# Kernel tuning notes

Measured on AMD Instinct MI355X. Metric: run time of the kernel, lower is better.

The kernel has to match this reference:

```python
import jax, jax.numpy as jnp
import numpy as np
import math

B, C, BINS, W = 2, 8, 1024, 512
HEADS = 16
HD = BINS // HEADS          # 64 head dim
ROT = BINS // HEADS // 2    # 32 rotated dims
EXP = 4
EPS = 1e-5
MAX_FREQ = 10.0


def setup_inputs() -> dict:
    key = jax.random.key(0)
    ks = jax.random.split(key, 8)
    def u(k, shape, fan_in):
        lim = 1.0 / math.sqrt(fan_in)
        return jax.random.uniform(k, shape, jnp.float32, -lim, lim)
    return {
        "x": jax.random.normal(ks[0], (B, C, BINS, W), jnp.float32),
        "norm1_w": jnp.ones((BINS,), jnp.float32),
        "norm1_b": jnp.zeros((BINS,), jnp.float32),
        # 'pixel' rotary init: linspace(1, max_freq/2, dim//2) * pi (learned)
        "rot_freqs": jnp.linspace(1.0, MAX_FREQ / 2, ROT // 2, dtype=jnp.float32) * math.pi,
        "q_w": u(ks[1], (C, BINS, BINS), BINS),
        "out_w": u(ks[2], (C, BINS, BINS), BINS),
        "norm2_w": jnp.ones((BINS,), jnp.float32),
        "norm2_b": jnp.zeros((BINS,), jnp.float32),
        "lin1_w": u(ks[3], (C, BINS * EXP, BINS), BINS),
        "lin2_w": u(ks[4], (C, BINS, BINS * EXP), BINS * EXP),
    }


def _mlin(x, w):
    # x: [b,c,f_in,w]; w: [c,f_out,f_in] -> [b,c,f_out,w]
    return jnp.einsum('bcfw,cgf->bcgw', x, w)


def _frame_norm(x, w, b):
    # LayerNorm over the bins axis (axis=2) of [b,c,bins,w]
    m = jnp.mean(x, axis=2, keepdims=True)
    v = jnp.var(x, axis=2, keepdims=True)
    xn = (x - m) * jax.lax.rsqrt(v + EPS)
    return xn * w[:, None] + b[:, None]


def _rotate(q, cos, sin):
    # q: [b,c,h,w,d]; rotate first ROT dims with interleaved-pair rotate_half
    q1, q2 = q[..., :ROT], q[..., ROT:]
    qp = q1.reshape(*q1.shape[:-1], ROT // 2, 2)
    rh = jnp.stack([-qp[..., 1], qp[..., 0]], axis=-1).reshape(q1.shape)
    return jnp.concatenate([q1 * cos + rh * sin, q2], axis=-1)


def _attention(x, rot_freqs, q_w, out_w):
    b, c, bins, w = x.shape
    # faithful to source: q, k, v ALL use q_proj
    y = _mlin(x, q_w)  # [b,c,bins,w]
    # -> [b,c,h,w,d]
    y = y.transpose(0, 1, 3, 2).reshape(b, c, w, HEADS, HD).transpose(0, 1, 3, 2, 4)
    # rotary angles: t * freqs, repeat-interleaved x2 -> [w, ROT]
    t = jnp.arange(w, dtype=jnp.float32)
    ang = jnp.repeat(t[:, None] * rot_freqs[None, :], 2, axis=-1)
    cos, sin = jnp.cos(ang), jnp.sin(ang)
    q = _rotate(y, cos, sin)
    k = _rotate(y, cos, sin)
    v = y
    # NOTE: source scales by 1/sqrt(h) where h == bins (spectral height)
    scores = jnp.einsum('bchwd,bchud->bchwu', q, k) / math.sqrt(bins)
    a = jnp.einsum('bchwu,bchud->bchwd', jax.nn.softmax(scores, axis=-1), v)
    # [b,c,h,w,d] -> [b,c,bins,w]
    a = a.transpose(0, 1, 3, 2, 4).reshape(b, c, w, bins).transpose(0, 1, 3, 2)
    return _mlin(a, out_w)


def reference(x, norm1_w, norm1_b, rot_freqs, q_w, out_w,
              norm2_w, norm2_b, lin1_w, lin2_w):
    z = _frame_norm(x, norm1_w, norm1_b)
    z = _attention(z, rot_freqs, q_w, out_w)
    x = x + z  # dropout=0 -> identity
    z = _frame_norm(x, norm2_w, norm2_b)
    z = _mlin(jax.nn.gelu(_mlin(z, lin1_w), approximate=False), lin2_w)
    return x + z
```

## Files before the change

kernel.cpp:

```cpp
#include <hip/hip_runtime.h>
#include <math.h>

#define BB 2
#define CCH 8
#define BINS 1024
#define WW 512
#define HEADS 16
#define HD 64
#define ROTD 32
#define EXPF 4
#define NXE 8388608L
#define NTW 32

typedef unsigned short ushortT;
typedef short bf16x8 __attribute__((ext_vector_type(8)));
typedef float f32x4 __attribute__((ext_vector_type(4)));

__device__ __forceinline__ ushortT f2bf(float f) {
    unsigned int u = __float_as_uint(f);
    u = (u + 0x7FFF + ((u >> 16) & 1)) >> 16;
    return (ushortT)u;
}
__device__ __forceinline__ float bf2f(ushortT h) {
    return __uint_as_float(((unsigned int)h) << 16);
}
__device__ __forceinline__ unsigned int cvtpk(float lo, float hi) {
    unsigned int r;
    asm("v_cvt_pk_bf16_f32 %0, %1, %2" : "=v"(r) : "v"(lo), "v"(hi));
    return r;
}
__device__ __forceinline__ float geluf(float x) {
    return 0.5f * x * (1.f + erff(x * 0.70710678118654752f));
}
__device__ __forceinline__ void gl_lds16(const ushortT* g, ushortT* l) {
    __builtin_amdgcn_global_load_lds(
        (const __attribute__((address_space(1))) unsigned int*)g,
        (__attribute__((address_space(3))) unsigned int*)l, 16, 0, 0);
}

__global__ __launch_bounds__(1024)
void normT_k(const float* __restrict__ X, const float* __restrict__ wgt,
             const float* __restrict__ bia, ushortT* __restrict__ YT)
{
    __shared__ float tile[NTW][BINS + 1];
    __shared__ float red0[32][NTW], red1[32][NTW];
    __shared__ float ms[NTW], is[NTW];
    const int bc = blockIdx.x >> 4;
    const int w0 = (blockIdx.x & 15) * NTW;
    const int tid = threadIdx.x;
    const int w  = tid & (NTW - 1);
    const int fy = tid >> 5;
    const float* Xb = X + (long)bc * BINS * WW + w0;
    float s = 0.f, s2 = 0.f;
    for (int f = fy; f < BINS; f += 32) {
        float v = Xb[(long)f * WW + w];
        s += v; s2 += v * v;
        tile[w][f] = v;
    }
    red0[fy][w] = s; red1[fy][w] = s2;
    __syncthreads();
    if (tid < NTW) {
        float ss = 0.f, qq = 0.f;
        #pragma unroll
        for (int j = 0; j < 32; ++j) { ss += red0[j][tid]; qq += red1[j][tid]; }
        float m = ss * (1.f / BINS);
        float var = qq * (1.f / BINS) - m * m;
        ms[tid] = m; is[tid] = rsqrtf(var + 1e-5f);
    }
    __syncthreads();
    const int w2 = tid >> 5;
    const int c  = tid & 31;
    float m = ms[w2], inv = is[w2];
    ushortT* Yb = YT + ((long)bc * WW + w0 + w2) * BINS;
    #pragma unroll
    for (int jj = 0; jj < 4; ++jj) {
        int f0 = jj * 256 + c * 8;
        union { ushortT h[8]; uint4 v; } r;
        #pragma unroll
        for (int e = 0; e < 8; ++e) {
            int f = f0 + e;
            float v = (tile[w2][f] - m) * inv * wgt[f] + bia[f];
            r.h[e] = f2bf(v);
        }
        *(uint4*)&Yb[f0] = r.v;
    }
}

__global__ void rope_tab_k(const float* __restrict__ freqs,
                           float* __restrict__ cosT, float* __restrict__ sinT)
{
    int idx = blockIdx.x * 256 + threadIdx.x;
    if (idx >= WW * 16) return;
    int w = idx >> 4, i = idx & 15;
    float ang = (float)w * freqs[i];
    cosT[idx] = cosf(ang);
    sinT[idx] = sinf(ang);
}

__global__ __launch_bounds__(256)
void mattn_k(const ushortT* __restrict__ rotT, const ushortT* __restrict__ yT,
             ushortT* __restrict__ oT)
{
    __shared__ ushortT Qs[64 * 64];
    __shared__ ushortT Ks[64 * 64];
    __shared__ ushortT Vs[64 * 72];
    __shared__ ushortT Ps[64 * 72];
    const int z = blockIdx.y;
    const int bc = z >> 4, h = z & 15;
    const int wq0 = blockIdx.x * 64;
    const int tid = threadIdx.x;
    const int wv = tid >> 6, l = tid & 63;
    const int lr = l & 15, lk = l >> 4;
    const long hbase = (long)bc * WW * 1024 + h * 64;

    #pragma unroll
    for (int p = 0; p < 2; ++p) {
        int r0 = p * 32 + wv * 8;
        int row = r0 + (l >> 3);
        int gs = (l & 7) ^ (row & 7);
        gl_lds16(rotT + hbase + (long)(wq0 + row) * 1024 + gs * 8, Qs + r0 * 64);
    }

    f32x4 oacc[4] = {};
    float mrow[4] = {-INFINITY, -INFINITY, -INFINITY, -INFINITY};
    float lrow[4] = {0.f, 0.f, 0.f, 0.f};

    for (int u0 = 0; u0 < WW; u0 += 64) {
        #pragma unroll
        for (int p = 0; p < 2; ++p) {
            int r0 = p * 32 + wv * 8;
            int row = r0 + (l >> 3);
            int gs = (l & 7) ^ (row & 7);
            gl_lds16(rotT + hbase + (long)(u0 + row) * 1024 + gs * 8, Ks + r0 * 64);
        }
        #pragma unroll
        for (int rep = 0; rep < 2; ++rep) {
            int ch = rep * 4 + wv;
            union { uint4 v; ushortT h8[8]; } tmp;
            tmp.v = *(const uint4*)(yT + hbase + (long)(u0 + l) * 1024 + ch * 8);
            #pragma unroll
            for (int j = 0; j < 8; ++j)
                Vs[(ch * 8 + j) * 72 + l] = tmp.h8[j];
        }
        __syncthreads();

        f32x4 sacc[4] = {};
        #pragma unroll
        for (int ko = 0; ko < 2; ++ko) {
            int ar = wv * 16 + lr;
            bf16x8 aq = *(const bf16x8*)&Qs[ar * 64 + (((ko * 4) + lk) ^ (ar & 7)) * 8];
            #pragma unroll
            for (int f = 0; f < 4; ++f) {
                int br = f * 16 + lr;
                bf16x8 bk = *(const bf16x8*)&Ks[br * 64 + (((ko * 4) + lk) ^ (br & 7)) * 8];
                sacc[f] = __builtin_amdgcn_mfma_f32_16x16x32_bf16(aq, bk, sacc[f], 0, 0, 0);
            }
        }

        #pragma unroll
        for (int rg = 0; rg < 4; ++rg) {
            float s0 = sacc[0][rg] * (1.f / 32.f);
            float s1 = sacc[1][rg] * (1.f / 32.f);
            float s2 = sacc[2][rg] * (1.f / 32.f);
            float s3 = sacc[3][rg] * (1.f / 32.f);
            float mx = fmaxf(fmaxf(s0, s1), fmaxf(s2, s3));
            mx = fmaxf(mx, __shfl_xor(mx, 1));
            mx = fmaxf(mx, __shfl_xor(mx, 2));
            mx = fmaxf(mx, __shfl_xor(mx, 4));
            mx = fmaxf(mx, __shfl_xor(mx, 8));
            float mnew = fmaxf(mrow[rg], mx);
            float al = __expf(mrow[rg] - mnew);
            float p0 = __expf(s0 - mnew), p1 = __expf(s1 - mnew);
            float p2 = __expf(s2 - mnew), p3 = __expf(s3 - mnew);
            float rs = p0 + p1 + p2 + p3;
            rs += __shfl_xor(rs, 1);
            rs += __shfl_xor(rs, 2);
            rs += __shfl_xor(rs, 4);
            rs += __shfl_xor(rs, 8);
            lrow[rg] = lrow[rg] * al + rs;
            mrow[rg] = mnew;
            oacc[0][rg] *= al; oacc[1][rg] *= al;
            oacc[2][rg] *= al; oacc[3][rg] *= al;
            int prow = wv * 16 + lk * 4 + rg;
            Ps[prow * 72 +  0 + lr] = f2bf(p0);
            Ps[prow * 72 + 16 + lr] = f2bf(p1);
            Ps[prow * 72 + 32 + lr] = f2bf(p2);
            Ps[prow * 72 + 48 + lr] = f2bf(p3);
        }
        asm volatile("s_waitcnt lgkmcnt(0)" ::: "memory");

        #pragma unroll
        for (int ko = 0; ko < 2; ++ko) {
            int ar = wv * 16 + lr;
            bf16x8 ap = *(const bf16x8*)&Ps[ar * 72 + ko * 32 + lk * 8];
            #pragma unroll
            for (int f = 0; f < 4; ++f) {
                bf16x8 bv = *(const bf16x8*)&Vs[(f * 16 + lr) * 72 + ko * 32 + lk * 8];
                oacc[f] = __builtin_amdgcn_mfma_f32_16x16x32_bf16(ap, bv, oacc[f], 0, 0, 0);
            }
        }
        __syncthreads();
    }

    #pragma unroll
    for (int rg = 0; rg < 4; ++rg) {
        float inv = 1.f / lrow[rg];
        int w = wq0 + wv * 16 + lk * 4 + rg;
        long b2 = (long)bc * WW * 1024 + (long)w * 1024 + h * 64;
        #pragma unroll
        for (int f = 0; f < 4; ++f)
            oT[b2 + f * 16 + lr] = f2bf(oacc[f][rg] * inv);
    }
}

template<bool HASRES, bool GELUF, bool TRANSOUT, bool ROPE>
__global__ __launch_bounds__(256)
void fgemm_k(const float* __restrict__ A, long sA, int aMod,
             const ushortT* __restrict__ B, long sB,
             void* __restrict__ Cp, long sC,
             const float* __restrict__ R, long sR,
             ushortT* __restrict__ Crot,
             const float* __restrict__ cosT, const float* __restrict__ sinT,
             int M, int N, int K, int gx, int gy)
{
    __shared__ ushortT smem[2 * 8192];
    ushortT* As = smem;
    ushortT* Bs = smem + 8192;
    const int nwg = gridDim.x;
    const int bid = blockIdx.x;
    const int lid = (bid & 7) * (nwg >> 3) + (bid >> 3);
    const int x = lid % gx;
    const int y = (lid / gx) % gy;
    const int z = lid / (gx * gy);
    const float*   Ab = A + (long)(z % aMod) * sA + (long)y * 128 * K;
    const ushortT* Bb = B + (long)z * sB + (long)x * 128 * K;
    const int tid = threadIdx.x;
    const int wv = tid >> 6, l = tid & 63;
    const int lrow = l & 15, lk = l >> 4;
    const int mb = (wv >> 1) * 64, nb = (wv & 1) * 64;
    const int arow = tid >> 3, agrp = tid & 7;
    f32x4 acc[4][4] = {};
    float4 a0[4], a1[4];
    const int NT = K >> 6;

    auto fetchA = [&](int k0) {
        #pragma unroll
        for (int c = 0; c < 4; ++c) {
            const float* src = Ab + (long)(arow + c * 32) * K + k0 + agrp * 8;
            a0[c] = *(const float4*)src;
            a1[c] = *(const float4*)(src + 4);
        }
    };
    auto commitA = [&]() {
        #pragma unroll
        for (int c = 0; c < 4; ++c) {
            int row = arow + c * 32;
            uint4 v;
            v.x = cvtpk(a0[c].x, a0[c].y);
            v.y = cvtpk(a0[c].z, a0[c].w);
            v.z = cvtpk(a1[c].x, a1[c].y);
            v.w = cvtpk(a1[c].z, a1[c].w);
            *(uint4*)&As[row * 64 + ((agrp ^ (row & 7)) << 3)] = v;
        }
    };
    auto stageB = [&](int k0) {
        #pragma unroll
        for (int t = 0; t < 4; ++t) {
            int r0 = wv * 32 + t * 8;
            int row = r0 + (l >> 3);
            int gs = (l & 7) ^ (row & 7);
            gl_lds16(Bb + (long)row * K + k0 + gs * 8, Bs + r0 * 64);
        }
    };
    auto compute = [&]() {
        #pragma unroll
        for (int ko = 0; ko < 2; ++ko) {
            bf16x8 af[4], bg[4];
            #pragma unroll
            for (int i = 0; i < 4; ++i) {
                int ra = mb + i * 16 + lrow;
                af[i] = *(const bf16x8*)&As[ra * 64 + ((lk + ko * 4) ^ (ra & 7)) * 8];
                int rb = nb + i * 16 + lrow;
                bg[i] = *(const bf16x8*)&Bs[rb * 64 + ((lk + ko * 4) ^ (rb & 7)) * 8];
            }
            #pragma unroll
            for (int i = 0; i < 4; ++i)
                #pragma unroll
                for (int j = 0; j < 4; ++j)
                    acc[i][j] = __builtin_amdgcn_mfma_f32_16x16x32_bf16(
                        af[i], bg[j], acc[i][j], 0, 0, 0);
        }
    };

    fetchA(0);
    for (int t = 0; t < NT; ++t) {
        if (t > 0) __syncthreads();
        stageB(t << 6);
        commitA();
        if (t + 1 < NT) fetchA((t + 1) << 6);
        __syncthreads();
        compute();
    }

    const int m0g = y * 128 + mb, n0g = x * 128 + nb;
    if (!TRANSOUT) {
        float* Cf = (float*)Cp + (long)z * sC;
        #pragma unroll
        for (int i = 0; i < 4; ++i)
            #pragma unroll
            for (int j = 0; j < 4; ++j)
                #pragma unroll
                for (int rg = 0; rg < 4; ++rg) {
                    long m = m0g + i * 16 + lk * 4 + rg;
                    long n = n0g + j * 16 + lrow;
                    float v = acc[i][j][rg];
                    if (GELUF) v = geluf(v);
                    if (HASRES) v += R[(long)z * sR + m * N + n];
                    Cf[m * N + n] = v;
                }
    } else {
        ushortT* Ts = smem + wv * 4096;
        __syncthreads();
        #pragma unroll
        for (int i = 0; i < 4; ++i)
            #pragma unroll
            for (int j = 0; j < 4; ++j)
                #pragma unroll
                for (int rg = 0; rg < 4; ++rg) {
                    int ml = i * 16 + lk * 4 + rg;
                    int nl = j * 16 + lrow;
                    float v = acc[i][j][rg];
                    if (GELUF) v = geluf(v);
                    Ts[nl * 64 + (((ml >> 3) ^ (nl & 7)) << 3) + (ml & 7)] = f2bf(v);
                }
        __syncthreads();
        ushortT* CT = (ushortT*)Cp + (long)z * sC;
        #pragma unroll
        for (int p = 0; p < 8; ++p) {
            int nl = p * 8 + (l >> 3), mc = l & 7;
            uint4 d = *(const uint4*)&Ts[nl * 64 + ((mc ^ (nl & 7)) << 3)];
            int wg = n0g + nl;
            int g0 = m0g + mc * 8;
            *(uint4*)&CT[(long)wg * M + g0] = d;
            if (ROPE) {
                ushortT* RT = Crot + (long)z * sC;
                int d0 = g0 & 63;
                if (d0 >= ROTD) {
                    *(uint4*)&RT[(long)wg * M + g0] = d;
                } else {
                    union { uint4 v; ushortT h8[8]; } in, ov;
                    in.v = d;
                    #pragma unroll
                    for (int j = 0; j < 8; j += 2) {
                        int i2 = (d0 + j) >> 1;
                        float cc = cosT[wg * 16 + i2], ss = sinT[wg * 16 + i2];
                        float a = bf2f(in.h8[j]), b = bf2f(in.h8[j + 1]);
                        ov.h8[j]     = f2bf(a * cc - b * ss);
                        ov.h8[j + 1] = f2bf(b * cc + a * ss);
                    }
                    *(uint4*)&RT[(long)wg * M + g0] = ov.v;
                }
            }
        }
    }
}

extern "C" void kernel_launch(void* const* d_in, const int* in_sizes, int n_in,
                              void* d_out, int out_size, void* d_ws, size_t ws_size,
                              hipStream_t stream)
{
    const float* x    = (const float*)d_in[0];
    const float* n1w  = (const float*)d_in[1];
    const float* n1b  = (const float*)d_in[2];
    const float* freqs= (const float*)d_in[3];
    const float* qw   = (const float*)d_in[4];
    const float* ow   = (const float*)d_in[5];
    const float* n2w  = (const float*)d_in[6];
    const float* n2b  = (const float*)d_in[7];
    const float* l1w  = (const float*)d_in[8];
    const float* l2w  = (const float*)d_in[9];
    float* out = (float*)d_out;
    char* wsb  = (char*)d_ws;
    const long MB = 1L << 20;

    ushortT* znT  = (ushortT*)(wsb +   0 * MB);
    ushortT* yT   = (ushortT*)(wsb +  16 * MB);
    ushortT* rotT = (ushortT*)(wsb +  32 * MB);
    ushortT* CfT  = (ushortT*)(wsb +  48 * MB);
    ushortT* zn2T = (ushortT*)(wsb +  64 * MB);
    ushortT* h1T  = (ushortT*)(wsb +  80 * MB);
    float*   cosT = (float*)  (wsb + 144 * MB);
    float*   sinT = cosT + WW * 16;

    rope_tab_k<<<32, 256, 0, stream>>>(freqs, cosT, sinT);

    normT_k<<<BB * CCH * 16, 1024, 0, stream>>>(x, n1w, n1b, znT);

    fgemm_k<false, false, true, true><<<512, 256, 0, stream>>>(
        qw,  (long)BINS * BINS, CCH,
        znT, (long)WW * BINS,
        yT,  (long)WW * BINS,
        nullptr, 0,
        rotT, cosT, sinT,
        BINS, WW, BINS, 4, 8);

    mattn_k<<<dim3(8, 256), 256, 0, stream>>>(rotT, yT, CfT);

    fgemm_k<true, false, false, false><<<512, 256, 0, stream>>>(
        ow,  (long)BINS * BINS, CCH,
        CfT, (long)WW * BINS,
        out, (long)BINS * WW,
        x,   (long)BINS * WW,
        nullptr, nullptr, nullptr,
        BINS, WW, BINS, 4, 8);

    normT_k<<<BB * CCH * 16, 1024, 0, stream>>>(out, n2w, n2b, zn2T);

    fgemm_k<false, true, true, false><<<2048, 256, 0, stream>>>(
        l1w,  (long)BINS * EXPF * BINS, CCH,
        zn2T, (long)WW * BINS,
        h1T,  (long)WW * BINS * EXPF,
        nullptr, 0,
        nullptr, nullptr, nullptr,
        BINS * EXPF, WW, BINS, 4, 32);

    fgemm_k<true, false, false, false><<<512, 256, 0, stream>>>(
        l2w, (long)BINS * BINS * EXPF, CCH,
        h1T, (long)WW * BINS * EXPF,
        out, (long)BINS * WW,
        out, (long)BINS * WW,
        nullptr, nullptr, nullptr,
        BINS, WW, BINS * EXPF, 4, 8);
}
```

Measured before the change: 439.2 us.

## Add dedicated lin1 GEMM kernel with 128x512 tiles and swizzled LDS

Replaces the generic fgemm launch for the lin1 expansion GEMM with a specialised kernel that uses 512-thread blocks computing a 128x512 output tile, with the full W dimension per block. Weights are fetched as fp32, converted to bf16 and register-prefetched one step ahead, while activations are staged by direct global-to-LDS loads into XOR-swizzled shared memory. GELU and the transposed bf16 store go through an LDS transpose so that global writes are coalesced. The goal is more reuse of each weight tile and fewer blocks, at the cost of higher register pressure (128 accumulators per thread) and single-buffered LDS with two barriers per k-step.

```diff
diff --git a/kernel.cpp b/kernel.cpp
--- a/kernel.cpp
+++ b/kernel.cpp
@@ -210,6 +210,117 @@
         #pragma unroll
         for (int f = 0; f < 4; ++f)
             oT[b2 + f * 16 + lr] = f2bf(oacc[f][rg] * inv);
+    }
+}
+
+__global__ __launch_bounds__(512)
+void lin1_k(const float* __restrict__ A, const ushortT* __restrict__ B,
+            ushortT* __restrict__ C)
+{
+    __shared__ ushortT smem[(128 + 512) * 64];
+    ushortT* As = smem;
+    ushortT* Bs = smem + 128 * 64;
+    const int bid = blockIdx.x;
+    const int lid = (bid & 7) * 64 + (bid >> 3);
+    const int y = lid & 31;
+    const int z = lid >> 5;
+    const float* Ab = A + (long)(z & 7) * 4096 * 1024 + (long)y * 128 * 1024;
+    const ushortT* Bb = B + (long)z * 512 * 1024;
+    const int tid = threadIdx.x;
+    const int wv = tid >> 6, l = tid & 63;
+    const int lrow = l & 15, lk = l >> 4;
+    const int rbase = (wv >> 2) * 64;
+    const int cbase = (wv & 3) * 128;
+    const int arow = tid >> 2, ag0 = (tid & 3) * 2;
+    f32x4 acc[2][4][4] = {};
+    float4 av[4];
+
+    auto fetchA = [&](int k0) {
+        const float* src = Ab + (long)arow * 1024 + k0 + ag0 * 8;
+        av[0] = *(const float4*)src;
+        av[1] = *(const float4*)(src + 4);
+        av[2] = *(const float4*)(src + 8);
+        av[3] = *(const float4*)(src + 12);
+    };
+    auto commitA = [&]() {
+        uint4 v0, v1;
+        v0.x = cvtpk(av[0].x, av[0].y); v0.y = cvtpk(av[0].z, av[0].w);
+        v0.z = cvtpk(av[1].x, av[1].y); v0.w = cvtpk(av[1].z, av[1].w);
+        v1.x = cvtpk(av[2].x, av[2].y); v1.y = cvtpk(av[2].z, av[2].w);
+        v1.z = cvtpk(av[3].x, av[3].y); v1.w = cvtpk(av[3].z, av[3].w);
+        *(uint4*)&As[arow * 64 + ((ag0 ^ (arow & 7)) << 3)] = v0;
+        *(uint4*)&As[arow * 64 + (((ag0 + 1) ^ (arow & 7)) << 3)] = v1;
+    };
+    auto stageB = [&](int k0) {
+        #pragma unroll
+        for (int p = 0; p < 8; ++p) {
+            int r0 = p * 64 + wv * 8;
+            int row = r0 + (l >> 3);
+            int gs = (l & 7) ^ (row & 7);
+            gl_lds16(Bb + (long)row * 1024 + k0 + gs * 8, Bs + r0 * 64);
+        }
+    };
+    auto compute = [&]() {
+        #pragma unroll
+        for (int ko = 0; ko < 2; ++ko) {
+            bf16x8 af[4], bg[2][4];
+            #pragma unroll
+            for (int i = 0; i < 4; ++i) {
+                int ra = rbase + i * 16 + lrow;
+                af[i] = *(const bf16x8*)&As[ra * 64 + ((lk + ko * 4) ^ (ra & 7)) * 8];
+            }
+            #pragma unroll
+            for (int s = 0; s < 2; ++s)
+                #pragma unroll
+                for (int j = 0; j < 4; ++j) {
+                    int rb = cbase + s * 64 + j * 16 + lrow;
+                    bg[s][j] = *(const bf16x8*)&Bs[rb * 64 + ((lk + ko * 4) ^ (rb & 7)) * 8];
+                }
+            #pragma unroll
+            for (int s = 0; s < 2; ++s)
+                #pragma unroll
+                for (int i = 0; i < 4; ++i)
+                    #pragma unroll
+                    for (int j = 0; j < 4; ++j)
+                        acc[s][i][j] = __builtin_amdgcn_mfma_f32_16x16x32_bf16(
+                            af[i], bg[s][j], acc[s][i][j], 0, 0, 0);
+        }
+    };
+
+    fetchA(0);
+    for (int t = 0; t < 16; ++t) {
+        if (t > 0) __syncthreads();
+        stageB(t << 6);
+        commitA();
+        if (t < 15) fetchA((t + 1) << 6);
+        __syncthreads();
+        compute();
+    }
+
+    __syncthreads();
+    ushortT* Ts = smem + wv * 4096;
+    const int m0g = y * 128 + rbase;
+    ushortT* Cz = C + (long)z * 512 * 4096;
+    #pragma unroll
+    for (int s = 0; s < 2; ++s) {
+        #pragma unroll
+        for (int i = 0; i < 4; ++i)
+            #pragma unroll
+            for (int j = 0; j < 4; ++j)
+                #pragma unroll
+                for (int rg = 0; rg < 4; ++rg) {
+                    int ml = i * 16 + lk * 4 + rg;
+                    int nl = j * 16 + lrow;
+                    Ts[nl * 64 + (((ml >> 3) ^ (nl & 7)) << 3) + (ml & 7)] =
+                        f2bf(geluf(acc[s][i][j][rg]));
+                }
+        #pragma unroll
+        for (int p = 0; p < 8; ++p) {
+            int nl = p * 8 + (l >> 3), mc = l & 7;
+            uint4 d = *(const uint4*)&Ts[nl * 64 + ((mc ^ (nl & 7)) << 3)];
+            int wg = cbase + s * 64 + nl;
+            *(uint4*)&Cz[(long)wg * 4096 + m0g + mc * 8] = d;
+        }
     }
 }
 
@@ -416,13 +527,7 @@
 
     normT_k<<<BB * CCH * 16, 1024, 0, stream>>>(out, n2w, n2b, zn2T);
 
-    fgemm_k<false, true, true, false><<<2048, 256, 0, stream>>>(
-        l1w,  (long)BINS * EXPF * BINS, CCH,
-        zn2T, (long)WW * BINS,
-        h1T,  (long)WW * BINS * EXPF,
-        nullptr, 0,
-        nullptr, nullptr, nullptr,
-        BINS * EXPF, WW, BINS, 4, 32);
+    lin1_k<<<512, 512, 0, stream>>>(l1w, zn2T, h1T);
 
     fgemm_k<true, false, false, false><<<512, 256, 0, stream>>>(
         l2w, (long)BINS * BINS * EXPF, CCH,
```

After: 466.4 us. 6.2% more time.

## Pre-cast MLP weights to bf16 and use a triple-buffered LDS-pipelined GEMM

Applied to the files above, without the earlier changes.

Adds a kernel that converts the fp32 lin1/lin2 weights to bf16 in workspace before each MLP GEMM. A new 128x256-tile, 512-thread GEMM then streams both operands straight into LDS through global_load_lds with XOR swizzling and a three-stage prefetch pipeline. This replaces the fp32-weight GEMM path, which loaded and converted the weights inside the kernel. The cost is two extra full passes over the weights each call, plus reuse of the znT workspace region for the bf16 weights.

```diff
diff --git a/kernel.cpp b/kernel.cpp
--- a/kernel.cpp
+++ b/kernel.cpp
@@ -36,6 +36,19 @@
     __builtin_amdgcn_global_load_lds(
         (const __attribute__((address_space(1))) unsigned int*)g,
         (__attribute__((address_space(3))) unsigned int*)l, 16, 0, 0);
+}
+
+__global__ __launch_bounds__(256)
+void wcast_k(const float* __restrict__ s, ushortT* __restrict__ d, long n)
+{
+    long i = ((long)blockIdx.x * 256 + threadIdx.x) * 8;
+    if (i >= n) return;
+    float4 a = *(const float4*)&s[i];
+    float4 b = *(const float4*)&s[i + 4];
+    uint4 v;
+    v.x = cvtpk(a.x, a.y); v.y = cvtpk(a.z, a.w);
+    v.z = cvtpk(b.x, b.y); v.w = cvtpk(b.z, b.w);
+    *(uint4*)&d[i] = v;
 }
 
 __global__ __launch_bounds__(1024)
@@ -213,6 +226,135 @@
     }
 }
 
+template<bool HASRES, bool GELUF, bool TRANSOUT>
+__global__ __launch_bounds__(512)
+void pgemm_k(const ushortT* __restrict__ A, long sA, int aMod,
+             const ushortT* __restrict__ B, long sB,
+             void* __restrict__ Cp, long sC,
+             const float* __restrict__ R, long sR,
+             int M, int N, int K, int gx, int gy)
+{
+    __shared__ ushortT smem[3 * 24576];
+    const int nwg = gridDim.x;
+    const int bid = blockIdx.x;
+    const int lid = (bid & 7) * (nwg >> 3) + (bid >> 3);
+    const int x = lid % gx;
+    const int y = (lid / gx) % gy;
+    const int z = lid / (gx * gy);
+    const ushortT* Ab = A + (long)(z % aMod) * sA + (long)y * 128 * K;
+    const ushortT* Bb = B + (long)z * sB + (long)x * 256 * K;
+    const int tid = threadIdx.x;
+    const int wv = tid >> 6, l = tid & 63;
+    const int lrow = l & 15, lk = l >> 4;
+    const int mb = (wv >> 2) * 64;
+    const int nb = (wv & 3) * 64;
+    f32x4 acc[4][4] = {};
+    const int NT = K >> 6;
+
+    auto stage = [&](int T) {
+        ushortT* S = smem + (T % 3) * 24576;
+        ushortT* As = S;
+        ushortT* Bs = S + 8192;
+        const int k0 = T << 6;
+        #pragma unroll
+        for (int t = 0; t < 2; ++t) {
+            int r0 = wv * 16 + t * 8;
+            int row = r0 + (l >> 3);
+            int gs = (l & 7) ^ (row & 7);
+            gl_lds16(Ab + (long)row * K + k0 + gs * 8, As + r0 * 64);
+        }
+        #pragma unroll
+        for (int t = 0; t < 4; ++t) {
+            int r0 = wv * 32 + t * 8;
+            int row = r0 + (l >> 3);
+            int gs = (l & 7) ^ (row & 7);
+            gl_lds16(Bb + (long)row * K + k0 + gs * 8, Bs + r0 * 64);
+        }
+    };
+    auto compute = [&](int T) {
+        const ushortT* S = smem + (T % 3) * 24576;
+        const ushortT* As = S;
+        const ushortT* Bs = S + 8192;
+        #pragma unroll
+        for (int ko = 0; ko < 2; ++ko) {
+            bf16x8 af[4], bg[4];
+            #pragma unroll
+            for (int i = 0; i < 4; ++i) {
+                int ra = mb + i * 16 + lrow;
+                af[i] = *(const bf16x8*)&As[ra * 64 + ((lk + ko * 4) ^ (ra & 7)) * 8];
+                int rb = nb + i * 16 + lrow;
+                bg[i] = *(const bf16x8*)&Bs[rb * 64 + ((lk + ko * 4) ^ (rb & 7)) * 8];
+            }
+            #pragma unroll
+            for (int i = 0; i < 4; ++i)
+                #pragma unroll
+                for (int j = 0; j < 4; ++j)
+                    acc[i][j] = __builtin_amdgcn_mfma_f32_16x16x32_bf16(
+                        af[i], bg[j], acc[i][j], 0, 0, 0);
+        }
+    };
+
+    stage(0);
+    if (NT > 1) {
+        stage(1);
+        asm volatile("s_waitcnt vmcnt(6)" ::: "memory");
+    } else {
+        asm volatile("s_waitcnt vmcnt(0)" ::: "memory");
+    }
+    __builtin_amdgcn_s_barrier();
+
+    for (int T = 0; T < NT; ++T) {
+        if (T + 2 < NT) stage(T + 2);
+        compute(T);
+        if (T + 1 < NT) {
+            if (T + 2 < NT) asm volatile("s_waitcnt vmcnt(6)" ::: "memory");
+            else            asm volatile("s_waitcnt vmcnt(0)" ::: "memory");
+            __builtin_amdgcn_s_barrier();
+        }
+    }
+
+    const int m0g = y * 128 + mb, n0g = x * 256 + nb;
+    if (!TRANSOUT) {
+        float* Cf = (float*)Cp + (long)z * sC;
+        #pragma unroll
+        for (int i = 0; i < 4; ++i)
+            #pragma unroll
+            for (int j = 0; j < 4; ++j)
+                #pragma unroll
+                for (int rg = 0; rg < 4; ++rg) {
+                    long m = m0g + i * 16 + lk * 4 + rg;
+                    long n = n0g + j * 16 + lrow;
+                    float v = acc[i][j][rg];
+                    if (GELUF) v = geluf(v);
+                    if (HASRES) v += R[(long)z * sR + m * N + n];
+                    Cf[m * N + n] = v;
+                }
+    } else {
+        __syncthreads();
+        ushortT* Ts = smem + wv * 4096;
+        #pragma unroll
+        for (int i = 0; i < 4; ++i)
+            #pragma unroll
+            for (int j = 0; j < 4; ++j)
+                #pragma unroll
+                for (int rg = 0; rg < 4; ++rg) {
+                    int ml = i * 16 + lk * 4 + rg;
+                    int nl = j * 16 + lrow;
+                    float v = acc[i][j][rg];
+                    if (GELUF) v = geluf(v);
+                    Ts[nl * 64 + (((ml >> 3) ^ (nl & 7)) << 3) + (ml & 7)] = f2bf(v);
+                }
+        __syncthreads();
+        ushortT* CT = (ushortT*)Cp + (long)z * sC;
+        #pragma unroll
+        for (int p = 0; p < 8; ++p) {
+            int nl = p * 8 + (l >> 3), mc = l & 7;
+            uint4 d = *(const uint4*)&Ts[nl * 64 + ((mc ^ (nl & 7)) << 3)];
+            *(uint4*)&CT[(long)(n0g + nl) * M + m0g + mc * 8] = d;
+        }
+    }
+}
+
 template<bool HASRES, bool GELUF, bool TRANSOUT, bool ROPE>
 __global__ __launch_bounds__(256)
 void fgemm_k(const float* __restrict__ A, long sA, int aMod,
@@ -387,6 +529,7 @@
     ushortT* yT   = (ushortT*)(wsb +  16 * MB);
     ushortT* rotT = (ushortT*)(wsb +  32 * MB);
     ushortT* CfT  = (ushortT*)(wsb +  48 * MB);
+    ushortT* wB   = (ushortT*)(wsb +   0 * MB);
     ushortT* zn2T = (ushortT*)(wsb +  64 * MB);
     ushortT* h1T  = (ushortT*)(wsb +  80 * MB);
     float*   cosT = (float*)  (wsb + 144 * MB);
@@ -414,21 +557,23 @@
         nullptr, nullptr, nullptr,
         BINS, WW, BINS, 4, 8);
 
+    wcast_k<<<16384, 256, 0, stream>>>(l1w, wB, 8L * BINS * EXPF * BINS);
+
     normT_k<<<BB * CCH * 16, 1024, 0, stream>>>(out, n2w, n2b, zn2T);
 
-    fgemm_k<false, true, true, false><<<2048, 256, 0, stream>>>(
-        l1w,  (long)BINS * EXPF * BINS, CCH,
+    pgemm_k<false, true, true><<<1024, 512, 0, stream>>>(
+        wB,   (long)BINS * EXPF * BINS, CCH,
         zn2T, (long)WW * BINS,
         h1T,  (long)WW * BINS * EXPF,
         nullptr, 0,
-        nullptr, nullptr, nullptr,
-        BINS * EXPF, WW, BINS, 4, 32);
-
-    fgemm_k<true, false, false, false><<<512, 256, 0, stream>>>(
-        l2w, (long)BINS * BINS * EXPF, CCH,
+        BINS * EXPF, WW, BINS, 2, 32);
+
+    wcast_k<<<16384, 256, 0, stream>>>(l2w, wB, 8L * BINS * EXPF * BINS);
+
+    pgemm_k<true, false, false><<<256, 512, 0, stream>>>(
+        wB,  (long)BINS * BINS * EXPF, CCH,
         h1T, (long)WW * BINS * EXPF,
         out, (long)BINS * WW,
         out, (long)BINS * WW,
-        nullptr, nullptr, nullptr,
-        BINS, WW, BINS * EXPF, 4, 8);
-}
+        BINS, WW, BINS * EXPF, 2, 8);
+}
```

Result: no change. 434.5 us (-1.1%).
